# Performance work log

Measured on AMD Instinct MI355X. Metric: run time of the kernel, lower is better.

## Reference

```python
import jax, jax.numpy as jnp
import numpy as np

DAMPENING = 50.0
THR = 1.0
TAU = 10.0
DECAY = float(np.exp(-1.0 / TAU))
V_MIN = -1.0


@jax.custom_vjp
def spike_fn(v_scaled):
    # Heaviside spike with surrogate (triangular) gradient
    return (v_scaled > 0.0).astype(v_scaled.dtype)

def _spike_fwd(v_scaled):
    return spike_fn(v_scaled), v_scaled

def _spike_bwd(v_scaled, dy):
    return (dy * DAMPENING * jnp.maximum(0.0, 1.0 - jnp.abs(v_scaled)),)

spike_fn.defvjp(_spike_fwd, _spike_bwd)


def setup_inputs() -> dict:
    key = jax.random.key(0)
    T, B, N_IN, N = 256, 32, 256, 2048
    ks = jax.random.split(key, 4)
    x = jax.random.normal(ks[0], (T, B, N_IN), jnp.float32)
    W_in = jax.random.normal(ks[1], (N_IN, N), jnp.float32) * (1.0 / np.sqrt(N_IN))
    b = jnp.zeros((N,), jnp.float32)
    # original uses stddev 1/sqrt(n_in) for Bernoulli_weights as well
    W_bern = jax.random.normal(ks[2], (N, N), jnp.float32) * (1.0 / np.sqrt(N_IN))
    random_indices = jax.random.randint(ks[3], (T, N), 0, N)
    return {"x": x, "W_in": W_in, "b": b, "W_bern": W_bern,
            "random_indices": random_indices}


def reference(x, W_in, b, W_bern, random_indices):
    # x: [T, B, n_in]; states v, z2: [B, n]
    B, N = x.shape[1], W_in.shape[1]
    v0 = jnp.zeros((B, N), x.dtype)
    z2_0 = jnp.zeros((B, N), x.dtype)  # old_spike state (unused in math, as in original)

    def step(carry, inp):
        v, _old_z2 = carry
        xt, idx = inp
        i_in = xt @ W_in + b                               # [B, n]
        new_v = jnp.clip(DECAY * v + i_in, V_MIN, THR + 0.01)
        z = spike_fn(new_v - THR)                          # spikes [B, n]
        new_v = jnp.where(z > 0.0, V_MIN, new_v)           # hard reset
        z2 = jnp.take(z @ W_bern, idx, axis=1)             # stochastic projection + column gather
        return (new_v, z2), (z, new_v, z2)

    _, (zs, vs, z2s) = jax.lax.scan(step, (v0, z2_0), (x, random_indices))
    return jnp.stack([zs, vs, z2s], axis=0)  # [3, T, B, n]
```

## Files before the change

kernel.cpp:

```cpp
#include <hip/hip_runtime.h>
#include <hip/hip_bf16.h>
#include <stdint.h>


#define T_STEPS 256
#define BATCH   32
#define NIN     256
#define NN      2048
#define BN_FLAT (BATCH * NN)
#define TBN     (T_STEPS * BATCH * NN)
#define MROWS   (T_STEPS * BATCH)

typedef __attribute__((ext_vector_type(4))) float fx4;
typedef __attribute__((ext_vector_type(4))) int   ix4;

__device__ __forceinline__ void gll16(const void* g, void* l) {
  typedef __attribute__((address_space(1))) void gvoid_t;
  typedef __attribute__((address_space(3))) void lvoid_t;
  __builtin_amdgcn_global_load_lds((gvoid_t*)(g), (lvoid_t*)(l), 16, 0, 0);
}

__device__ __forceinline__ void mfma16(fx4& d, ix4 a, ix4 b) {
  asm volatile("v_mfma_f32_16x16x32_bf16 %0, %1, %2, %0" : "+v"(d) : "v"(a), "v"(b));
}

__global__ __launch_bounds__(256) void xt_k(const float* __restrict__ X,
                                            float* __restrict__ Xt) {
  __shared__ float tile[32][33];
  const int m0 = blockIdx.x << 5, k0 = blockIdx.y << 5;
  const int tx = threadIdx.x, ty = threadIdx.y;
#pragma unroll
  for (int i = 0; i < 32; i += 8)
    tile[ty + i][tx] = X[(size_t)(m0 + ty + i) * NIN + k0 + tx];
  __syncthreads();
#pragma unroll
  for (int i = 0; i < 32; i += 8)
    Xt[(size_t)(k0 + ty + i) * MROWS + m0 + tx] = tile[tx][ty + i];
}

__global__ __launch_bounds__(256) void wt_convert(const float* __restrict__ W,
                                                  __hip_bfloat16* __restrict__ Wt) {
  __shared__ float tile[32][33];
  const int k0 = blockIdx.y << 5, n0 = blockIdx.x << 5;
  const int tx = threadIdx.x, ty = threadIdx.y;
#pragma unroll
  for (int i = 0; i < 32; i += 8)
    tile[ty + i][tx] = W[(size_t)(k0 + ty + i) * NN + n0 + tx];
  __syncthreads();
#pragma unroll
  for (int i = 0; i < 32; i += 8)
    Wt[(size_t)(n0 + ty + i) * NN + k0 + tx] = __float2bfloat16(tile[tx][ty + i]);
}

__global__ __launch_bounds__(256, 2) void in_gemm(const float* __restrict__ Xt,
                                                  const float* __restrict__ Wi,
                                                  const float* __restrict__ bias,
                                                  float* __restrict__ I) {
  __shared__ __align__(16) float As[16 * 256];
  __shared__ __align__(16) float Bs[16 * 128];
  const int tid = threadIdx.x;
  const int lane = tid & 63;
  const int w = tid >> 6;
  const int tm = tid >> 4;
  const int tn = tid & 15;
  const int m0 = blockIdx.x * 256, n0 = blockIdx.y * 128;

  fx4 acc[16][2] = {};

  const char* gA = (const char*)(Xt + (size_t)(w * 4) * MROWS + m0 + lane * 4);
  char* lA = (char*)As + w * 4096 + lane * 16;
  const char* gB = (const char*)(Wi + (size_t)(w * 4 + (lane >> 5)) * NN + n0 + (lane & 31) * 4);
  char* lB = (char*)Bs + w * 2048 + lane * 16;

  for (int k0 = 0; k0 < NIN; k0 += 16) {
#pragma unroll
    for (int i = 0; i < 4; ++i) gll16(gA + (size_t)i * (MROWS * 4), lA + i * 1024);
#pragma unroll
    for (int j = 0; j < 2; ++j) gll16(gB + (size_t)j * (2 * NN * 4), lB + j * 1024);
    gA += (size_t)16 * MROWS * 4;
    gB += (size_t)16 * NN * 4;
    __syncthreads();
#pragma unroll
    for (int kk = 0; kk < 16; ++kk) {
      fx4 av[4], bv[2];
#pragma unroll
      for (int q = 0; q < 4; ++q) av[q] = *(const fx4*)&As[kk * 256 + tm * 16 + q * 4];
      bv[0] = *(const fx4*)&Bs[kk * 128 + tn * 4];
      bv[1] = *(const fx4*)&Bs[kk * 128 + 64 + tn * 4];
#pragma unroll
      for (int r = 0; r < 16; ++r) {
        const float a = av[r >> 2][r & 3];
#pragma unroll
        for (int j = 0; j < 2; ++j)
#pragma unroll
          for (int c = 0; c < 4; ++c)
            acc[r][j][c] = fmaf(a, bv[j][c], acc[r][j][c]);
      }
    }
    __syncthreads();
  }

#pragma unroll
  for (int r = 0; r < 16; ++r) {
    const size_t row = (size_t)(m0 + tm * 16 + r) * NN;
    fx4 r0, r1;
#pragma unroll
    for (int c = 0; c < 4; ++c) {
      r0[c] = acc[r][0][c] + bias[n0 + tn * 4 + c];
      r1[c] = acc[r][1][c] + bias[n0 + 64 + tn * 4 + c];
    }
    *(fx4*)&I[row + n0 + tn * 4] = r0;
    *(fx4*)&I[row + n0 + 64 + tn * 4] = r1;
  }
}

__device__ __forceinline__ void scan_body(float* zs, float* vsout,
                                          const float* I, __hip_bfloat16* Zb) {
  const int nid = blockIdx.x * 256 + threadIdx.x;
  float v = 0.f;
  for (int t0 = 0; t0 < T_STEPS; t0 += 8) {
    float iin[8];
#pragma unroll
    for (int u = 0; u < 8; ++u)
      iin[u] = I[(size_t)(t0 + u) * BN_FLAT + nid];
#pragma unroll
    for (int u = 0; u < 8; ++u) {
      float nv = __fadd_rn(__fmul_rn(0.9048374180359595f, v), iin[u]);
      nv = fminf(fmaxf(nv, -1.0f), 1.01f);
      const bool sp = nv > 1.0f;
      const float z = sp ? 1.0f : 0.0f;
      nv = sp ? -1.0f : nv;
      const size_t off = (size_t)(t0 + u) * BN_FLAT + nid;
      zs[off] = z;
      vsout[off] = nv;
      Zb[off] = __float2bfloat16(z);
      v = nv;
    }
  }
}

__global__ __launch_bounds__(256) void scan_sep(float* __restrict__ out,
                                                const float* __restrict__ I,
                                                __hip_bfloat16* __restrict__ Zb) {
  scan_body(out, out + (size_t)TBN, I, Zb);
}

__global__ __launch_bounds__(256) void scan_inp(float* out, __hip_bfloat16* Zb) {
  scan_body(out, out + (size_t)TBN, out + (size_t)TBN, Zb);
}

__global__ __launch_bounds__(256) void bern_gemm(const __hip_bfloat16* __restrict__ Z,
                                                 const __hip_bfloat16* __restrict__ Wt,
                                                 float* __restrict__ Y) {
  __shared__ __align__(16) __hip_bfloat16 Asm[128 * 32];
  __shared__ __align__(16) __hip_bfloat16 Bsm[128 * 32];
  const int tid = threadIdx.x;
  const int lane = tid & 63;
  const int wid = tid >> 6;
  const int wr = wid >> 1, wc = wid & 1;
  const int m0 = blockIdx.x * 128, n0 = blockIdx.y * 128;

  fx4 acc[4][4] = {};

  const int trow = tid >> 2;
  const int tcol = (tid & 3) << 4;
  const char* gA = (const char*)Z + ((size_t)(m0 + trow) << 12) + tcol;
  const char* gB = (const char*)Wt + ((size_t)(n0 + trow) << 12) + tcol;
  char* lA = (char*)Asm + tid * 16;
  char* lB = (char*)Bsm + tid * 16;

  const ix4* Au = (const ix4*)Asm;
  const ix4* Bu = (const ix4*)Bsm;
  const int abase = (wr * 64 + (lane & 15)) * 4 + (lane >> 4);
  const int bbase = (wc * 64 + (lane & 15)) * 4 + (lane >> 4);

  for (int ks = 0; ks < 64; ++ks) {
    gll16(gA, lA);
    gll16(gA + (size_t)64 * 4096, lA + 4096);
    gll16(gB, lB);
    gll16(gB + (size_t)64 * 4096, lB + 4096);
    gA += 64;
    gB += 64;
    __syncthreads();

    ix4 af[4], bf[4];
#pragma unroll
    for (int i = 0; i < 4; ++i) af[i] = Au[abase + i * 64];
#pragma unroll
    for (int i = 0; i < 4; ++i) bf[i] = Bu[bbase + i * 64];
#pragma unroll
    for (int mf = 0; mf < 4; ++mf)
#pragma unroll
      for (int nf = 0; nf < 4; ++nf)
        mfma16(acc[mf][nf], af[mf], bf[nf]);
    __syncthreads();
  }

  asm volatile("s_nop 7\n\ts_nop 7");

  const int crow = (lane >> 4) * 4;
  const int ccol = lane & 15;
#pragma unroll
  for (int mf = 0; mf < 4; ++mf)
#pragma unroll
    for (int nf = 0; nf < 4; ++nf)
#pragma unroll
      for (int j = 0; j < 4; ++j) {
        const int r = m0 + wr * 64 + mf * 16 + crow + j;
        const int c = n0 + wc * 64 + nf * 16 + ccol;
        Y[(size_t)r * NN + c] = acc[mf][nf][j];
      }
}

__global__ __launch_bounds__(256) void gather_k(float* __restrict__ Y,
                                                const int* __restrict__ ridx) {
  __shared__ __align__(16) float rowbuf[NN];
  const int tb = blockIdx.x;
  const int t = tb >> 5;
  float* yrow = Y + (size_t)tb * NN;
  const int tid = threadIdx.x;
#pragma unroll
  for (int i = 0; i < 2; ++i) {
    int u = tid + i * 256;
    ((fx4*)rowbuf)[u] = ((const fx4*)yrow)[u];
  }
  __syncthreads();
  const int* ir = ridx + t * NN;
#pragma unroll
  for (int i = 0; i < 8; ++i) {
    int j = tid + i * 256;
    yrow[j] = rowbuf[ir[j]];
  }
}

extern "C" void kernel_launch(void* const* d_in, const int* in_sizes, int n_in,
                              void* d_out, int out_size, void* d_ws, size_t ws_size,
                              hipStream_t stream) {
  const float* x      = (const float*)d_in[0];
  const float* W_in   = (const float*)d_in[1];
  const float* bias   = (const float*)d_in[2];
  const float* W_bern = (const float*)d_in[3];
  const int*   ridx   = (const int*)d_in[4];
  float* out = (float*)d_out;
  char* ws = (char*)d_ws;

  __hip_bfloat16* Wt = (__hip_bfloat16*)ws;
  __hip_bfloat16* Zb = (__hip_bfloat16*)(ws + (size_t)8388608);
  const size_t offI = 41943040;
  const bool sep = ws_size >= (size_t)109051904;
  float* Ibuf = sep ? (float*)(ws + offI) : (out + (size_t)TBN);

  float* Xt = out;

  xt_k<<<dim3(256, 8), dim3(32, 8), 0, stream>>>(x, Xt);
  wt_convert<<<dim3(64, 64), dim3(32, 8), 0, stream>>>(W_bern, Wt);
  in_gemm<<<dim3(32, 16), dim3(256), 0, stream>>>(Xt, W_in, bias, Ibuf);
  if (sep)
    scan_sep<<<dim3(256), dim3(256), 0, stream>>>(out, Ibuf, Zb);
  else
    scan_inp<<<dim3(256), dim3(256), 0, stream>>>(out, Zb);
  bern_gemm<<<dim3(64, 16), dim3(256), 0, stream>>>(Zb, Wt, out + (size_t)2 * TBN);
  gather_k<<<dim3(8192), dim3(256), 0, stream>>>(out + (size_t)2 * TBN, ridx);
}
```

Baseline: 252.3 us.

## Double-buffer input GEMM LDS tiles and shrink M tile to 128

```diff
diff --git a/kernel.cpp b/kernel.cpp
--- a/kernel.cpp
+++ b/kernel.cpp
@@ -52,57 +52,70 @@
     Wt[(size_t)(n0 + ty + i) * NN + k0 + tx] = __float2bfloat16(tile[tx][ty + i]);
 }
 
-__global__ __launch_bounds__(256, 2) void in_gemm(const float* __restrict__ Xt,
-                                                  const float* __restrict__ Wi,
-                                                  const float* __restrict__ bias,
-                                                  float* __restrict__ I) {
-  __shared__ __align__(16) float As[16 * 256];
-  __shared__ __align__(16) float Bs[16 * 128];
+__global__ __launch_bounds__(256) void in_gemm(const float* __restrict__ Xt,
+                                               const float* __restrict__ Wi,
+                                               const float* __restrict__ bias,
+                                               float* __restrict__ I) {
+  __shared__ __align__(16) float As[2][16 * 128];
+  __shared__ __align__(16) float Bs[2][16 * 128];
   const int tid = threadIdx.x;
-  const int lane = tid & 63;
-  const int w = tid >> 6;
   const int tm = tid >> 4;
   const int tn = tid & 15;
-  const int m0 = blockIdx.x * 256, n0 = blockIdx.y * 128;
-
-  fx4 acc[16][2] = {};
-
-  const char* gA = (const char*)(Xt + (size_t)(w * 4) * MROWS + m0 + lane * 4);
-  char* lA = (char*)As + w * 4096 + lane * 16;
-  const char* gB = (const char*)(Wi + (size_t)(w * 4 + (lane >> 5)) * NN + n0 + (lane & 31) * 4);
-  char* lB = (char*)Bs + w * 2048 + lane * 16;
-
-  for (int k0 = 0; k0 < NIN; k0 += 16) {
-#pragma unroll
-    for (int i = 0; i < 4; ++i) gll16(gA + (size_t)i * (MROWS * 4), lA + i * 1024);
-#pragma unroll
-    for (int j = 0; j < 2; ++j) gll16(gB + (size_t)j * (2 * NN * 4), lB + j * 1024);
-    gA += (size_t)16 * MROWS * 4;
-    gB += (size_t)16 * NN * 4;
-    __syncthreads();
-#pragma unroll
-    for (int kk = 0; kk < 16; ++kk) {
-      fx4 av[4], bv[2];
-#pragma unroll
-      for (int q = 0; q < 4; ++q) av[q] = *(const fx4*)&As[kk * 256 + tm * 16 + q * 4];
-      bv[0] = *(const fx4*)&Bs[kk * 128 + tn * 4];
-      bv[1] = *(const fx4*)&Bs[kk * 128 + 64 + tn * 4];
-#pragma unroll
-      for (int r = 0; r < 16; ++r) {
-        const float a = av[r >> 2][r & 3];
-#pragma unroll
-        for (int j = 0; j < 2; ++j)
-#pragma unroll
-          for (int c = 0; c < 4; ++c)
-            acc[r][j][c] = fmaf(a, bv[j][c], acc[r][j][c]);
-      }
-    }
-    __syncthreads();
-  }
-
-#pragma unroll
-  for (int r = 0; r < 16; ++r) {
-    const size_t row = (size_t)(m0 + tm * 16 + r) * NN;
+  const int m0 = blockIdx.x * 128, n0 = blockIdx.y * 128;
+
+  fx4 acc[8][2] = {};
+
+  const int srow = tid >> 5;
+  const int scol = (tid & 31) * 4;
+  const float* gA = Xt + (size_t)srow * MROWS + m0 + scol;
+  const float* gB = Wi + (size_t)srow * NN + n0 + scol;
+
+#define STAGE_IG(bi)                                                  \
+  do {                                                                \
+    gll16(gA, (char*)As[bi] + tid * 16);                              \
+    gll16(gA + 8 * MROWS, (char*)As[bi] + tid * 16 + 4096);           \
+    gll16(gB, (char*)Bs[bi] + tid * 16);                              \
+    gll16(gB + 8 * NN, (char*)Bs[bi] + tid * 16 + 4096);              \
+    gA += (size_t)16 * MROWS;                                         \
+    gB += (size_t)16 * NN;                                            \
+  } while (0)
+
+#define COMPUTE_IG(bi)                                                \
+  do {                                                                \
+    _Pragma("unroll") for (int kk = 0; kk < 16; ++kk) {               \
+      const float* ar = &As[bi][kk * 128 + tm * 8];                   \
+      const float* br = &Bs[bi][kk * 128 + tn * 4];                   \
+      fx4 a0 = *(const fx4*)ar, a1 = *(const fx4*)(ar + 4);           \
+      fx4 b0 = *(const fx4*)br, b1 = *(const fx4*)(br + 64);          \
+      _Pragma("unroll") for (int r = 0; r < 4; ++r) {                 \
+        _Pragma("unroll") for (int c = 0; c < 4; ++c) {               \
+          acc[r][0][c] = fmaf(a0[r], b0[c], acc[r][0][c]);            \
+          acc[r][1][c] = fmaf(a0[r], b1[c], acc[r][1][c]);            \
+          acc[r + 4][0][c] = fmaf(a1[r], b0[c], acc[r + 4][0][c]);    \
+          acc[r + 4][1][c] = fmaf(a1[r], b1[c], acc[r + 4][1][c]);    \
+        }                                                             \
+      }                                                               \
+    }                                                                 \
+  } while (0)
+
+  STAGE_IG(0);
+  for (int t = 0; t < 15; ++t) {
+    STAGE_IG((t + 1) & 1);
+    asm volatile("s_waitcnt vmcnt(4)" ::: "memory");
+    __builtin_amdgcn_s_barrier();
+    COMPUTE_IG(t & 1);
+    __builtin_amdgcn_s_barrier();
+  }
+  asm volatile("s_waitcnt vmcnt(0)" ::: "memory");
+  __builtin_amdgcn_s_barrier();
+  COMPUTE_IG(1);
+
+#undef STAGE_IG
+#undef COMPUTE_IG
+
+#pragma unroll
+  for (int r = 0; r < 8; ++r) {
+    const size_t row = (size_t)(m0 + tm * 8 + r) * NN;
     fx4 r0, r1;
 #pragma unroll
     for (int c = 0; c < 4; ++c) {
@@ -254,7 +267,7 @@
 
   xt_k<<<dim3(256, 8), dim3(32, 8), 0, stream>>>(x, Xt);
   wt_convert<<<dim3(64, 64), dim3(32, 8), 0, stream>>>(W_bern, Wt);
-  in_gemm<<<dim3(32, 16), dim3(256), 0, stream>>>(Xt, W_in, bias, Ibuf);
+  in_gemm<<<dim3(64, 16), dim3(256), 0, stream>>>(Xt, W_in, bias, Ibuf);
   if (sep)
     scan_sep<<<dim3(256), dim3(256), 0, stream>>>(out, Ibuf, Zb);
   else
```

After: 305.3 us. +21.0%, slower.
